# Kernel optimization log

Measured on AMD Instinct MI355X. Metric: run time of the kernel, lower is better.

The kernel has to match this reference:

```python
import jax, jax.numpy as jnp
import numpy as np

B, S, D = 2, 2048, 1024
H, DQK, DV = 16, 64, 64

def setup_inputs() -> dict:
    key = jax.random.key(0)
    k1, k2, k3, k4, k5 = jax.random.split(key, 5)
    scale_in = 1.0 / np.sqrt(D)
    scale_v = 1.0 / np.sqrt(H * DV)
    return {
        "x":   jax.random.normal(k1, (B, S, D), dtype=jnp.float32),
        "W_q": jax.random.uniform(k2, (D, H * DQK), minval=-scale_in, maxval=scale_in, dtype=jnp.float32),
        "W_k": jax.random.uniform(k3, (D, H * DQK), minval=-scale_in, maxval=scale_in, dtype=jnp.float32),
        "W_v": jax.random.uniform(k4, (D, H * DV), minval=-scale_in, maxval=scale_in, dtype=jnp.float32),
        "W_o": jax.random.uniform(k5, (H * DV, D), minval=-scale_v, maxval=scale_v, dtype=jnp.float32),
    }

def reference(x, W_q, W_k, W_v, W_o):
    b, s, _ = x.shape
    # projections -> [B, H, S, d]
    Q = (x @ W_q).reshape(b, s, H, DQK).transpose(0, 2, 1, 3)
    K = (x @ W_k).reshape(b, s, H, DQK).transpose(0, 2, 1, 3)
    V = (x @ W_v).reshape(b, s, H, DV).transpose(0, 2, 1, 3)
    scores = jnp.einsum('bhqd,bhkd->bhqk', Q, K) / np.sqrt(DQK).astype(np.float32)
    causal_mask = jnp.triu(jnp.ones((s, s), dtype=bool), k=1)  # True above diagonal
    scores = jnp.where(causal_mask[None, None], -jnp.inf, scores)
    attn = jax.nn.softmax(scores, axis=-1)
    out = jnp.einsum('bhqk,bhkd->bhqd', attn, V)  # [B,H,S,DV]
    out = out.transpose(0, 2, 1, 3).reshape(b, s, H * DV)
    return out @ W_o
```

## Files before the change

### kernel.cpp

```cpp
#include <hip/hip_runtime.h>


typedef float  f32x4  __attribute__((ext_vector_type(4)));
typedef __bf16 bf16x8 __attribute__((ext_vector_type(8)));

__device__ __forceinline__ unsigned short f2bf(float f) {
    __bf16 h = (__bf16)f;
    return __builtin_bit_cast(unsigned short, h);
}

__device__ __forceinline__ void gld16(unsigned short* lds, const unsigned short* g) {
    __builtin_amdgcn_global_load_lds(
        (const __attribute__((address_space(1))) void*)g,
        (__attribute__((address_space(3))) void*)lds, 16, 0, 0);
}

__global__ __launch_bounds__(256) void castx(const float* __restrict__ x,
                                             unsigned short* __restrict__ xb) {
    size_t i = ((size_t)blockIdx.x * 256 + threadIdx.x) * 4;
    float4 v = *(const float4*)(x + i);
    ushort4 o;
    o.x = f2bf(v.x); o.y = f2bf(v.y); o.z = f2bf(v.z); o.w = f2bf(v.w);
    *(ushort4*)(xb + i) = o;
}

__global__ __launch_bounds__(256) void wtrans(const float* __restrict__ W0,
                                              const float* __restrict__ W1,
                                              const float* __restrict__ W2,
                                              const float* __restrict__ W3,
                                              unsigned short* __restrict__ WT) {
    __shared__ float T[64][65];
    const int z = blockIdx.z;
    const float* W = (z == 0) ? W0 : (z == 1) ? W1 : (z == 2) ? W2 : W3;
    const int k0 = blockIdx.y * 64, n0 = blockIdx.x * 64;
    const int tid = threadIdx.x;
#pragma unroll
    for (int i = 0; i < 4; i++) {
        int c = tid + i * 256;
        int r = c >> 4, col = (c & 15) * 4;
        float4 v = *(const float4*)(W + (size_t)(k0 + r) * 1024 + n0 + col);
        T[r][col] = v.x; T[r][col + 1] = v.y; T[r][col + 2] = v.z; T[r][col + 3] = v.w;
    }
    __syncthreads();
    unsigned short* out = WT + (size_t)z * 1024 * 1024;
#pragma unroll
    for (int i = 0; i < 2; i++) {
        int c = tid + i * 256;
        int nr = c >> 3, koff = (c & 7) * 8;
        union { unsigned short us[8]; uint4 v; } pk;
#pragma unroll
        for (int j = 0; j < 8; j++) pk.us[j] = f2bf(T[koff + j][nr]);
        *(uint4*)(out + (size_t)(n0 + nr) * 1024 + k0 + koff) = pk.v;
    }
}

__global__ __launch_bounds__(256) void gemm_qkv(const unsigned short* __restrict__ A,
                                                const unsigned short* __restrict__ WTall,
                                                unsigned short* __restrict__ outq,
                                                unsigned short* __restrict__ Vp) {
    __shared__ unsigned short As[128 * 32];
    __shared__ unsigned short Bs[128 * 32];
    const int tid = threadIdx.x;
    const int w = tid >> 6, lane = tid & 63, quad = lane >> 4, ln = lane & 15;

    const int blk = blockIdx.x;
    const int n0 = ((blk >> 3) & 7) * 128;
    const int g  = ((blk >> 6) << 3) | (blk & 7);
    const int z  = g >> 5;
    const int m0 = (g & 31) * 128;

    const unsigned short* BT = WTall + (size_t)z * (1024 * 1024);
    const float scl = (z == 0) ? 0.180336878f : 1.0f;
    const bool swp = (z < 2);

    const int lr = lane >> 2;
    const int lc = ((lane & 3) ^ (lr & 3)) * 8;
    const int fsw = (quad ^ (ln & 3)) * 8;

    const f32x4 z4 = {0.f, 0.f, 0.f, 0.f};
    f32x4 acc[4][4];
#pragma unroll
    for (int i = 0; i < 4; i++)
#pragma unroll
        for (int j = 0; j < 4; j++) acc[i][j] = z4;

    const int wm = (w & 1) * 64, wn = (w >> 1) * 64;
    const int R0 = w * 32, R1 = w * 32 + 16;

    for (int k0 = 0; k0 < 1024; k0 += 32) {
        __syncthreads();
        gld16(As + R0 * 32, A  + (size_t)(m0 + R0 + lr) * 1024 + k0 + lc);
        gld16(As + R1 * 32, A  + (size_t)(m0 + R1 + lr) * 1024 + k0 + lc);
        gld16(Bs + R0 * 32, BT + (size_t)(n0 + R0 + lr) * 1024 + k0 + lc);
        gld16(Bs + R1 * 32, BT + (size_t)(n0 + R1 + lr) * 1024 + k0 + lc);
        __syncthreads();
        bf16x8 af[4], bfr[4];
#pragma unroll
        for (int t = 0; t < 4; t++)
            af[t] = *(const bf16x8*)&As[(wm + t * 16 + ln) * 32 + fsw];
#pragma unroll
        for (int t = 0; t < 4; t++)
            bfr[t] = *(const bf16x8*)&Bs[(wn + t * 16 + ln) * 32 + fsw];
        if (swp) {
#pragma unroll
            for (int tm = 0; tm < 4; tm++)
#pragma unroll
                for (int tn = 0; tn < 4; tn++)
                    acc[tm][tn] = __builtin_amdgcn_mfma_f32_16x16x32_bf16(
                        bfr[tn], af[tm], acc[tm][tn], 0, 0, 0);
        } else {
#pragma unroll
            for (int tm = 0; tm < 4; tm++)
#pragma unroll
                for (int tn = 0; tn < 4; tn++)
                    acc[tm][tn] = __builtin_amdgcn_mfma_f32_16x16x32_bf16(
                        af[tm], bfr[tn], acc[tm][tn], 0, 0, 0);
        }
    }

    if (swp) {
#pragma unroll
        for (int tm = 0; tm < 4; tm++)
#pragma unroll
            for (int tn = 0; tn < 4; tn++) {
                int mg = m0 + wm + tm * 16 + ln;
                int nb = n0 + wn + tn * 16 + quad * 4;
                int b = mg >> 11, s = mg & 2047, h = nb >> 6, dd = nb & 63;
                ushort4 o;
                o.x = f2bf(acc[tm][tn][0] * scl);
                o.y = f2bf(acc[tm][tn][1] * scl);
                o.z = f2bf(acc[tm][tn][2] * scl);
                o.w = f2bf(acc[tm][tn][3] * scl);
                size_t zoff = (size_t)z * (4096 * 1024);
                *(ushort4*)(outq + zoff + (((size_t)(b * 16 + h) * 2048 + s) << 6) + dd) = o;
            }
    } else {
#pragma unroll
        for (int tm = 0; tm < 4; tm++)
#pragma unroll
            for (int tn = 0; tn < 4; tn++) {
                int mg = m0 + wm + tm * 16 + quad * 4;
                int ng = n0 + wn + tn * 16 + ln;
                int b = mg >> 11, h = ng >> 6, dd = ng & 63;
                int sblk = (mg & 2047) & ~63;
                int cb = tm >> 1, t16 = tm & 1;
                int pp = cb * 32 + quad * 8 + t16 * 4;
                ushort4 o;
                o.x = f2bf(acc[tm][tn][0]);
                o.y = f2bf(acc[tm][tn][1]);
                o.z = f2bf(acc[tm][tn][2]);
                o.w = f2bf(acc[tm][tn][3]);
                *(ushort4*)(Vp + ((size_t)(b * 16 + h) * 64 + dd) * 2048 + sblk + pp) = o;
            }
    }
}

__global__ __launch_bounds__(256) void gemm_o(const unsigned short* __restrict__ A,
                                              const unsigned short* __restrict__ BT,
                                              float* __restrict__ outf) {
    __shared__ unsigned short As[128 * 32];
    __shared__ unsigned short Bs[128 * 32];
    const int tid = threadIdx.x;
    const int w = tid >> 6, lane = tid & 63, quad = lane >> 4, ln = lane & 15;

    const int blk = blockIdx.x;
    const int n0 = ((blk >> 3) & 7) * 128;
    const int m0 = (((blk >> 6) << 3) | (blk & 7)) * 128;

    const int lr = lane >> 2;
    const int lc = ((lane & 3) ^ (lr & 3)) * 8;
    const int fsw = (quad ^ (ln & 3)) * 8;

    const f32x4 z4 = {0.f, 0.f, 0.f, 0.f};
    f32x4 acc[4][4];
#pragma unroll
    for (int i = 0; i < 4; i++)
#pragma unroll
        for (int j = 0; j < 4; j++) acc[i][j] = z4;

    const int wm = (w & 1) * 64, wn = (w >> 1) * 64;
    const int R0 = w * 32, R1 = w * 32 + 16;

    for (int k0 = 0; k0 < 1024; k0 += 32) {
        __syncthreads();
        gld16(As + R0 * 32, A  + (size_t)(m0 + R0 + lr) * 1024 + k0 + lc);
        gld16(As + R1 * 32, A  + (size_t)(m0 + R1 + lr) * 1024 + k0 + lc);
        gld16(Bs + R0 * 32, BT + (size_t)(n0 + R0 + lr) * 1024 + k0 + lc);
        gld16(Bs + R1 * 32, BT + (size_t)(n0 + R1 + lr) * 1024 + k0 + lc);
        __syncthreads();
        bf16x8 af[4], bfr[4];
#pragma unroll
        for (int t = 0; t < 4; t++)
            af[t] = *(const bf16x8*)&As[(wm + t * 16 + ln) * 32 + fsw];
#pragma unroll
        for (int t = 0; t < 4; t++)
            bfr[t] = *(const bf16x8*)&Bs[(wn + t * 16 + ln) * 32 + fsw];
#pragma unroll
        for (int tm = 0; tm < 4; tm++)
#pragma unroll
            for (int tn = 0; tn < 4; tn++)
                acc[tm][tn] = __builtin_amdgcn_mfma_f32_16x16x32_bf16(
                    bfr[tn], af[tm], acc[tm][tn], 0, 0, 0);
    }

#pragma unroll
    for (int tm = 0; tm < 4; tm++)
#pragma unroll
        for (int tn = 0; tn < 4; tn++) {
            int mg = m0 + wm + tm * 16 + ln;
            int nb = n0 + wn + tn * 16 + quad * 4;
            *(f32x4*)(outf + (size_t)mg * 1024 + nb) = acc[tm][tn];
        }
}

__global__ __launch_bounds__(256, 4) void flash(const unsigned short* __restrict__ Qb,
                                                const unsigned short* __restrict__ Kb,
                                                const unsigned short* __restrict__ Vpb,
                                                unsigned short* __restrict__ AO) {
    __shared__ __align__(16) unsigned short Ks[2][64 * 64];
    __shared__ __align__(16) unsigned short Vs[2][64 * 64];
    const int tid = threadIdx.x, w = tid >> 6, lane = tid & 63;
    const int qd = lane >> 4, ln = lane & 15;
    const int lr = lane >> 3;
    const int lchunk = (lane & 7) ^ lr;
    const int psw = (qd ^ (ln & 7)) * 8;

    const int blk = blockIdx.x;
    const int pairid = blk >> 1;
    const int bh = pairid & 31;
    const int jj = pairid >> 5;
    const int qi = (blk & 1) ? jj : (31 - jj);
    const int qt0 = qi * 64;

    const unsigned short* Kg = Kb  + (size_t)bh * 2048 * 64;
    const unsigned short* Vg = Vpb + (size_t)bh * 64 * 2048;

    bf16x8 aq[2];
    {
        const unsigned short* Qrow = Qb + ((size_t)bh * 2048 + qt0 + w * 16 + ln) * 64 + qd * 8;
        aq[0] = *(const bf16x8*)(Qrow);
        aq[1] = *(const bf16x8*)(Qrow + 32);
    }

    const f32x4 z4 = {0.f, 0.f, 0.f, 0.f};
    f32x4 Oc[4];
#pragma unroll
    for (int td = 0; td < 4; td++) Oc[td] = z4;
    float lsum = 0.f;

    const int qrow = qt0 + w * 16 + ln;
    const int qmin = qt0 + w * 16;
    const int qmax = qmin + 15;
    const int kend = qt0 + 64;

#define FLASH_STAGE(buf, kk)                                                          \
    {                                                                                 \
        const unsigned short* kg = Kg + (size_t)((kk) + w * 16 + lr) * 64 + lchunk * 8; \
        gld16(&Ks[buf][(w * 16) * 64], kg);                                           \
        gld16(&Ks[buf][(w * 16 + 8) * 64], kg + 8 * 64);                              \
        const unsigned short* vg = Vg + (size_t)(w * 16 + lr) * 2048 + (kk) + lchunk * 8; \
        gld16(&Vs[buf][(w * 16) * 64], vg);                                           \
        gld16(&Vs[buf][(w * 16 + 8) * 64], vg + 8 * 2048);                            \
    }

    FLASH_STAGE(0, 0);
    int cur = 0;

    for (int k0 = 0; k0 < kend; k0 += 64) {
        __syncthreads();
        if (k0 + 64 < kend) FLASH_STAGE(cur ^ 1, k0 + 64);

        f32x4 sc[4];
#pragma unroll
        for (int t = 0; t < 4; t++) {
            sc[t] = z4;
            if (k0 + t * 16 <= qmax) {
                int off = (t * 16 + ln) * 64 + psw;
                bf16x8 bk0 = *(const bf16x8*)&Ks[cur][off];
                bf16x8 bk1 = *(const bf16x8*)&Ks[cur][off ^ 32];
                sc[t] = __builtin_amdgcn_mfma_f32_16x16x32_bf16(bk0, aq[0], sc[t], 0, 0, 0);
                sc[t] = __builtin_amdgcn_mfma_f32_16x16x32_bf16(bk1, aq[1], sc[t], 0, 0, 0);
            }
        }

        unsigned int pk[4][2];
#pragma unroll
        for (int t = 0; t < 4; t++) {
            if (k0 + t * 16 > qmax) { pk[t][0] = 0u; pk[t][1] = 0u; continue; }
            float e[4];
#pragma unroll
            for (int r = 0; r < 4; r++) e[r] = __builtin_amdgcn_exp2f(sc[t][r]);
            if (k0 + t * 16 + 15 > qmin) {
#pragma unroll
                for (int r = 0; r < 4; r++)
                    if (k0 + t * 16 + qd * 4 + r > qrow) e[r] = 0.f;
            }
            lsum += (e[0] + e[1]) + (e[2] + e[3]);
            pk[t][0] = (unsigned int)f2bf(e[0]) | ((unsigned int)f2bf(e[1]) << 16);
            pk[t][1] = (unsigned int)f2bf(e[2]) | ((unsigned int)f2bf(e[3]) << 16);
        }

        union { unsigned int u[4]; bf16x8 v; } apu0, apu1;
        apu0.u[0] = pk[0][0]; apu0.u[1] = pk[0][1]; apu0.u[2] = pk[1][0]; apu0.u[3] = pk[1][1];
        apu1.u[0] = pk[2][0]; apu1.u[1] = pk[2][1]; apu1.u[2] = pk[3][0]; apu1.u[3] = pk[3][1];
#pragma unroll
        for (int td = 0; td < 4; td++) {
            int voff = (td * 16 + ln) * 64 + psw;
            bf16x8 av0 = *(const bf16x8*)&Vs[cur][voff];
            bf16x8 av1 = *(const bf16x8*)&Vs[cur][voff ^ 32];
            Oc[td] = __builtin_amdgcn_mfma_f32_16x16x32_bf16(av0, apu0.v, Oc[td], 0, 0, 0);
            Oc[td] = __builtin_amdgcn_mfma_f32_16x16x32_bf16(av1, apu1.v, Oc[td], 0, 0, 0);
        }
        cur ^= 1;
    }
#undef FLASH_STAGE

    lsum += __shfl_xor(lsum, 16);
    lsum += __shfl_xor(lsum, 32);
    const float inv = 1.0f / lsum;

    const int bz = bh >> 4, h = bh & 15;
    const int rowg = qt0 + w * 16 + ln;
    unsigned short* aorow = AO + ((size_t)(bz * 2048 + rowg) << 10) + h * 64 + qd * 4;
#pragma unroll
    for (int td = 0; td < 4; td++) {
        ushort4 o;
        o.x = f2bf(Oc[td][0] * inv);
        o.y = f2bf(Oc[td][1] * inv);
        o.z = f2bf(Oc[td][2] * inv);
        o.w = f2bf(Oc[td][3] * inv);
        *(ushort4*)(aorow + td * 16) = o;
    }
}

extern "C" void kernel_launch(void* const* d_in, const int* in_sizes, int n_in,
                              void* d_out, int out_size, void* d_ws, size_t ws_size,
                              hipStream_t stream) {
    const float* x  = (const float*)d_in[0];
    const float* Wq = (const float*)d_in[1];
    const float* Wk = (const float*)d_in[2];
    const float* Wv = (const float*)d_in[3];
    const float* Wo = (const float*)d_in[4];
    float* out = (float*)d_out;

    unsigned short* xb  = (unsigned short*)d_ws;
    unsigned short* WT  = xb  + (size_t)4096 * 1024;
    unsigned short* Qb  = WT  + (size_t)4 * 1024 * 1024;
    unsigned short* Kb  = Qb  + (size_t)4096 * 1024;
    unsigned short* Vb  = Kb  + (size_t)4096 * 1024;
    unsigned short* Vpb = Vb  + (size_t)4096 * 1024;
    unsigned short* AO  = Vpb + (size_t)4096 * 1024;

    castx<<<4096, 256, 0, stream>>>(x, xb);
    wtrans<<<dim3(16, 16, 4), 256, 0, stream>>>(Wq, Wk, Wv, Wo, WT);
    gemm_qkv<<<dim3(768), 256, 0, stream>>>(xb, WT, Qb, Vpb);
    flash<<<dim3(1024), 256, 0, stream>>>(Qb, Kb, Vpb, AO);
    gemm_o<<<dim3(256), 256, 0, stream>>>(AO, WT + (size_t)3 * 1024 * 1024, out);
}
```

Before: 198.2 us.

## Double-buffer LDS tiles in QKV and output projection GEMMs

Both projection GEMMs now keep two LDS buffers for the A and B tiles. The loads for the next K-slice are issued before the MFMAs on the current slice, and each iteration has one barrier instead of two. The aim is to hide global-to-LDS latency behind matrix math. In exchange LDS use per block doubles to 32KB, and the overlap only holds if the compiler does not insert a conservative wait on the async LDS loads before the fragment reads.

```diff
diff --git a/kernel.cpp b/kernel.cpp
--- a/kernel.cpp
+++ b/kernel.cpp
@@ -58,8 +58,8 @@
                                                 const unsigned short* __restrict__ WTall,
                                                 unsigned short* __restrict__ outq,
                                                 unsigned short* __restrict__ Vp) {
-    __shared__ unsigned short As[128 * 32];
-    __shared__ unsigned short Bs[128 * 32];
+    __shared__ unsigned short As[2][128 * 32];
+    __shared__ unsigned short Bs[2][128 * 32];
     const int tid = threadIdx.x;
     const int w = tid >> 6, lane = tid & 63, quad = lane >> 4, ln = lane & 15;
 
@@ -87,20 +87,27 @@
     const int wm = (w & 1) * 64, wn = (w >> 1) * 64;
     const int R0 = w * 32, R1 = w * 32 + 16;
 
+#define QKV_STAGE(buf, kk)                                                         \
+    {                                                                              \
+        gld16(As[buf] + R0 * 32, A  + (size_t)(m0 + R0 + lr) * 1024 + (kk) + lc);  \
+        gld16(As[buf] + R1 * 32, A  + (size_t)(m0 + R1 + lr) * 1024 + (kk) + lc);  \
+        gld16(Bs[buf] + R0 * 32, BT + (size_t)(n0 + R0 + lr) * 1024 + (kk) + lc);  \
+        gld16(Bs[buf] + R1 * 32, BT + (size_t)(n0 + R1 + lr) * 1024 + (kk) + lc);  \
+    }
+
+    QKV_STAGE(0, 0);
+    int cur = 0;
+
     for (int k0 = 0; k0 < 1024; k0 += 32) {
         __syncthreads();
-        gld16(As + R0 * 32, A  + (size_t)(m0 + R0 + lr) * 1024 + k0 + lc);
-        gld16(As + R1 * 32, A  + (size_t)(m0 + R1 + lr) * 1024 + k0 + lc);
-        gld16(Bs + R0 * 32, BT + (size_t)(n0 + R0 + lr) * 1024 + k0 + lc);
-        gld16(Bs + R1 * 32, BT + (size_t)(n0 + R1 + lr) * 1024 + k0 + lc);
-        __syncthreads();
+        if (k0 + 32 < 1024) QKV_STAGE(cur ^ 1, k0 + 32);
         bf16x8 af[4], bfr[4];
 #pragma unroll
         for (int t = 0; t < 4; t++)
-            af[t] = *(const bf16x8*)&As[(wm + t * 16 + ln) * 32 + fsw];
+            af[t] = *(const bf16x8*)&As[cur][(wm + t * 16 + ln) * 32 + fsw];
 #pragma unroll
         for (int t = 0; t < 4; t++)
-            bfr[t] = *(const bf16x8*)&Bs[(wn + t * 16 + ln) * 32 + fsw];
+            bfr[t] = *(const bf16x8*)&Bs[cur][(wn + t * 16 + ln) * 32 + fsw];
         if (swp) {
 #pragma unroll
             for (int tm = 0; tm < 4; tm++)
@@ -116,7 +123,9 @@
                     acc[tm][tn] = __builtin_amdgcn_mfma_f32_16x16x32_bf16(
                         af[tm], bfr[tn], acc[tm][tn], 0, 0, 0);
         }
-    }
+        cur ^= 1;
+    }
+#undef QKV_STAGE
 
     if (swp) {
 #pragma unroll
@@ -158,8 +167,8 @@
 __global__ __launch_bounds__(256) void gemm_o(const unsigned short* __restrict__ A,
                                               const unsigned short* __restrict__ BT,
                                               float* __restrict__ outf) {
-    __shared__ unsigned short As[128 * 32];
-    __shared__ unsigned short Bs[128 * 32];
+    __shared__ unsigned short As[2][128 * 32];
+    __shared__ unsigned short Bs[2][128 * 32];
     const int tid = threadIdx.x;
     const int w = tid >> 6, lane = tid & 63, quad = lane >> 4, ln = lane & 15;
 
@@ -181,27 +190,36 @@
     const int wm = (w & 1) * 64, wn = (w >> 1) * 64;
     const int R0 = w * 32, R1 = w * 32 + 16;
 
+#define O_STAGE(buf, kk)                                                           \
+    {                                                                              \
+        gld16(As[buf] + R0 * 32, A  + (size_t)(m0 + R0 + lr) * 1024 + (kk) + lc);  \
+        gld16(As[buf] + R1 * 32, A  + (size_t)(m0 + R1 + lr) * 1024 + (kk) + lc);  \
+        gld16(Bs[buf] + R0 * 32, BT + (size_t)(n0 + R0 + lr) * 1024 + (kk) + lc);  \
+        gld16(Bs[buf] + R1 * 32, BT + (size_t)(n0 + R1 + lr) * 1024 + (kk) + lc);  \
+    }
+
+    O_STAGE(0, 0);
+    int cur = 0;
+
     for (int k0 = 0; k0 < 1024; k0 += 32) {
         __syncthreads();
-        gld16(As + R0 * 32, A  + (size_t)(m0 + R0 + lr) * 1024 + k0 + lc);
-        gld16(As + R1 * 32, A  + (size_t)(m0 + R1 + lr) * 1024 + k0 + lc);
-        gld16(Bs + R0 * 32, BT + (size_t)(n0 + R0 + lr) * 1024 + k0 + lc);
-        gld16(Bs + R1 * 32, BT + (size_t)(n0 + R1 + lr) * 1024 + k0 + lc);
-        __syncthreads();
+        if (k0 + 32 < 1024) O_STAGE(cur ^ 1, k0 + 32);
         bf16x8 af[4], bfr[4];
 #pragma unroll
         for (int t = 0; t < 4; t++)
-            af[t] = *(const bf16x8*)&As[(wm + t * 16 + ln) * 32 + fsw];
+            af[t] = *(const bf16x8*)&As[cur][(wm + t * 16 + ln) * 32 + fsw];
 #pragma unroll
         for (int t = 0; t < 4; t++)
-            bfr[t] = *(const bf16x8*)&Bs[(wn + t * 16 + ln) * 32 + fsw];
+            bfr[t] = *(const bf16x8*)&Bs[cur][(wn + t * 16 + ln) * 32 + fsw];
 #pragma unroll
         for (int tm = 0; tm < 4; tm++)
 #pragma unroll
             for (int tn = 0; tn < 4; tn++)
                 acc[tm][tn] = __builtin_amdgcn_mfma_f32_16x16x32_bf16(
                     bfr[tn], af[tm], acc[tm][tn], 0, 0, 0);
-    }
+        cur ^= 1;
+    }
+#undef O_STAGE
 
 #pragma unroll
     for (int tm = 0; tm < 4; tm++)
```

New measurement: 203.5 us. 2.7% more time.
